# Kernel tuning notes

Hardware: AMD Instinct MI355X
Metric: run time of the kernel (lower is better)

## Reference

```python
import jax, jax.numpy as jnp
import numpy as np

N = 50000      # nodes
E = 800000     # directed edges (before self-loops)
FEAT = 120     # raw node feature dim
TOPO = 8       # topological feature dim
H1, D1 = 8, 8  # conv1: heads, per-head dim
C = 40         # out_channels (classes)
NEG_SLOPE = 0.2


def setup_inputs() -> dict:
    key = jax.random.key(0)
    ks = jax.random.split(key, 10)
    return {
        "x": jax.random.normal(ks[0], (N, FEAT), dtype=jnp.float32),
        "topo": jax.random.normal(ks[1], (N, TOPO), dtype=jnp.float32),
        "edge_index": jax.random.randint(ks[2], (2, E), 0, N, dtype=jnp.int32),
        "W1": jax.random.normal(ks[3], (FEAT + TOPO, H1 * D1), dtype=jnp.float32) * 0.1,
        "a_src1": jax.random.normal(ks[4], (H1, D1), dtype=jnp.float32) * 0.1,
        "a_dst1": jax.random.normal(ks[5], (H1, D1), dtype=jnp.float32) * 0.1,
        "b1": jnp.zeros((H1 * D1,), dtype=jnp.float32),
        "W2": jax.random.normal(ks[6], (H1 * D1, C), dtype=jnp.float32) * 0.1,
        "a_src2": jax.random.normal(ks[7], (1, C), dtype=jnp.float32) * 0.1,
        "a_dst2": jax.random.normal(ks[8], (1, C), dtype=jnp.float32) * 0.1,
        "b2": jnp.zeros((C,), dtype=jnp.float32),
    }


def gat_conv(x, src, dst, W, a_src, a_dst, b, heads, d, concat):
    """PyG-style GATConv (eval mode). src/dst already include self-loops."""
    n = x.shape[0]
    h = (x @ W).reshape(n, heads, d)                      # [N,H,D]
    al_src = jnp.sum(h * a_src[None], axis=-1)            # [N,H]
    al_dst = jnp.sum(h * a_dst[None], axis=-1)            # [N,H]
    e = jax.nn.leaky_relu(al_src[src] + al_dst[dst], NEG_SLOPE)  # [E',H]
    # segment softmax over incoming edges per destination node
    m = jax.ops.segment_max(e, dst, num_segments=n)       # [N,H]
    p = jnp.exp(e - m[dst])                               # [E',H]
    s = jax.ops.segment_sum(p, dst, num_segments=n)       # [N,H]
    alpha = p / s[dst]                                    # [E',H]
    out = jax.ops.segment_sum(alpha[:, :, None] * h[src], dst, num_segments=n)  # [N,H,D]
    if concat:
        return out.reshape(n, heads * d) + b
    return out.mean(axis=1) + b


def reference(x, topo, edge_index, W1, a_src1, a_dst1, b1, W2, a_src2, a_dst2, b2):
    n = x.shape[0]
    loops = jnp.arange(n, dtype=edge_index.dtype)
    src = jnp.concatenate([edge_index[0], loops])
    dst = jnp.concatenate([edge_index[1], loops])
    xin = jnp.concatenate([x, topo], axis=1)              # [N, FEAT+TOPO]
    h = jax.nn.elu(gat_conv(xin, src, dst, W1, a_src1, a_dst1, b1, H1, D1, True))
    out = gat_conv(h, src, dst, W2, a_src2, a_dst2, b2, 1, C, False)
    return jax.nn.log_softmax(out, axis=1)
```

## Files before the change

kernel.cpp:

```cpp
#include <hip/hip_runtime.h>
#include <hip/hip_fp16.h>

#define NN 50000
#define EE 800000
#define NBUCK 196
#define CAP 5120
#define TILEA 2048
#define NBA ((EE + TILEA - 1) / TILEA)
#define NGB 782
#define SRCS_MAX (EE + 8 * NN + 64)
#define LOG2E 1.4426950408889634f
#define PF 6

typedef _Float16 half8 __attribute__((ext_vector_type(8)));
typedef float floatx4 __attribute__((ext_vector_type(4)));
typedef float floatx2 __attribute__((ext_vector_type(2)));

__device__ __forceinline__ unsigned char f32_to_fp8(float a) {
    int r = __builtin_amdgcn_cvt_pk_fp8_f32(a, a, 0, false);
    return (unsigned char)(r & 0xff);
}
__device__ __forceinline__ float2 fp8pair_lo(unsigned v) {
    floatx2 r = __builtin_amdgcn_cvt_pk_f32_fp8(v, false);
    return make_float2(r[0], r[1]);
}
__device__ __forceinline__ float2 fp8pair_hi(unsigned v) {
    floatx2 r = __builtin_amdgcn_cvt_pk_f32_fp8(v, true);
    return make_float2(r[0], r[1]);
}
__device__ __forceinline__ float fexp2(float x) {
#if __has_builtin(__builtin_amdgcn_exp2f)
    return __builtin_amdgcn_exp2f(x);
#else
    return exp2f(x);
#endif
}
__device__ __forceinline__ float fexp(float x) {
    return fexp2(x * LOG2E);
}
__device__ __forceinline__ float flog(float x) {
#if __has_builtin(__builtin_amdgcn_logf)
    return 0.6931471805599453f * __builtin_amdgcn_logf(x);
#else
    return __logf(x);
#endif
}
__device__ __forceinline__ float frcp(float x) {
#if __has_builtin(__builtin_amdgcn_rcpf)
    return __builtin_amdgcn_rcpf(x);
#else
    return 1.f / x;
#endif
}

__global__ void k_prep(const float* __restrict__ W1, const float* __restrict__ W2,
                       _Float16* __restrict__ Bf1, _Float16* __restrict__ Bf2,
                       int* __restrict__ cursor, float* __restrict__ al2s,
                       unsigned char* __restrict__ pk1, __half* __restrict__ h2p) {
    int tid = blockIdx.x * 256 + threadIdx.x;
    if (tid < 1024) {
        int kk = tid >> 8, ct = (tid >> 6) & 3, L = tid & 63;
        int k0 = kk * 32 + (L >> 4) * 8, col = ct * 16 + (L & 15);
        half8 v;
        #pragma unroll
        for (int j = 0; j < 8; j++) v[j] = (_Float16)W1[(k0 + j) * 64 + col];
        *(half8*)(Bf1 + ((size_t)((kk * 4 + ct) * 64 + L)) * 8) = v;
    } else if (tid < 1024 + 384) {
        int u = tid - 1024;
        int kk = u / 192, rem = u % 192;
        int ct = rem >> 6, L = rem & 63;
        int k0 = kk * 32 + (L >> 4) * 8, col = ct * 16 + (L & 15);
        half8 v;
        #pragma unroll
        for (int j = 0; j < 8; j++)
            v[j] = (col < 40) ? (_Float16)W2[(k0 + j) * 40 + col] : (_Float16)0.f;
        *(half8*)(Bf2 + ((size_t)((kk * 3 + ct) * 64 + L)) * 8) = v;
    } else {
        int u = tid - 1408;
        if (u < NBUCK) cursor[u] = 0;
        if (u == 208) al2s[NN] = -1e30f;
        if (u >= 216 && u < 236) ((unsigned*)(h2p + (size_t)NN * 40))[u - 216] = 0u;
        if (u >= 240 && u < 272) {
            int dw = u - 240;
            ((float*)(pk1 + (size_t)NN * 128))[dw] = ((dw & 3) == 0) ? -1e30f : 0.f;
        }
    }
}

__global__ __launch_bounds__(256) void k_fusedAG(
    const int* __restrict__ ei, int* __restrict__ cursor,
    unsigned* __restrict__ bucketData,
    const float* __restrict__ x, const float* __restrict__ topo,
    const _Float16* __restrict__ Bf1,
    const float* __restrict__ a_src, const float* __restrict__ a_dst,
    unsigned char* __restrict__ pk1, float* __restrict__ aldst) {
    if (blockIdx.x < NBA) {
        __shared__ int cnt[NBUCK], base[NBUCK];
        int t = threadIdx.x;
        for (int i = t; i < NBUCK; i += 256) cnt[i] = 0;
        __syncthreads();
        int e0 = blockIdx.x * TILEA;
        int nE = min(TILEA, EE - e0);
        unsigned pk[8]; int bk[8], rk[8];
        int m = 0;
        for (int i = t; i < nE; i += 256) {
            int e = e0 + i;
            int s = ei[e], d = ei[EE + e];
            pk[m] = ((unsigned)d << 16) | (unsigned)s;
            bk[m] = d >> 8;
            rk[m] = atomicAdd(&cnt[bk[m]], 1);
            m++;
        }
        __syncthreads();
        for (int i = t; i < NBUCK; i += 256)
            base[i] = (cnt[i] > 0) ? atomicAdd(&cursor[i], cnt[i]) : 0;
        __syncthreads();
        for (int k = 0; k < m; k++) {
            int pos = base[bk[k]] + rk[k];
            if (pos < CAP) bucketData[(size_t)bk[k] * CAP + pos] = pk[k];
        }
        return;
    }
    int wave = threadIdx.x >> 6, lane = threadIdx.x & 63;
    int row0 = (blockIdx.x - NBA) * 64 + wave * 16;
    if (row0 >= NN) return;
    int g = lane >> 4, li = lane & 15;
    int myrow = row0 + li;
    half8 B[16];
    const half8* bp = (const half8*)Bf1;
    #pragma unroll
    for (int i = 0; i < 16; i++) B[i] = bp[i * 64 + lane];
    floatx4 acc[4] = {{0,0,0,0},{0,0,0,0},{0,0,0,0},{0,0,0,0}};
    #pragma unroll
    for (int kk = 0; kk < 4; kk++) {
        int k0 = kk * 32 + g * 8;
        const float* sp = (k0 == 120) ? (topo + (size_t)myrow * 8)
                                      : (x + (size_t)myrow * 120 + k0);
        float4 u0 = ((const float4*)sp)[0];
        float4 u1 = ((const float4*)sp)[1];
        half8 av;
        av[0] = (_Float16)u0.x; av[1] = (_Float16)u0.y;
        av[2] = (_Float16)u0.z; av[3] = (_Float16)u0.w;
        av[4] = (_Float16)u1.x; av[5] = (_Float16)u1.y;
        av[6] = (_Float16)u1.z; av[7] = (_Float16)u1.w;
        #pragma unroll
        for (int ct = 0; ct < 4; ct++)
            acc[ct] = __builtin_amdgcn_mfma_f32_16x16x32_f16(av, B[kk * 4 + ct], acc[ct], 0, 0, 0);
    }
    #pragma unroll
    for (int ct = 0; ct < 4; ct++)
        #pragma unroll
        for (int r = 0; r < 4; r++) {
            int col = ct * 16 + li;
            pk1[(size_t)(row0 + 4 * g + r) * 128 + (((col >> 3) << 4) + 4 + (col & 7))]
                = f32_to_fp8(acc[ct][r]);
        }
    float ps[4][4], pd[4][4];
    #pragma unroll
    for (int ct = 0; ct < 4; ct++) {
        int head = 2 * ct + (li >> 3), dix = li & 7;
        float asv = a_src[head * 8 + dix];
        float adv = a_dst[head * 8 + dix];
        #pragma unroll
        for (int r = 0; r < 4; r++) {
            ps[ct][r] = acc[ct][r] * asv;
            pd[ct][r] = acc[ct][r] * adv;
        }
    }
    #pragma unroll
    for (int off = 1; off <= 4; off <<= 1)
        #pragma unroll
        for (int ct = 0; ct < 4; ct++)
            #pragma unroll
            for (int r = 0; r < 4; r++) {
                ps[ct][r] += __shfl_xor(ps[ct][r], off, 64);
                pd[ct][r] += __shfl_xor(pd[ct][r], off, 64);
            }
    if ((li & 7) == 0) {
        #pragma unroll
        for (int ct = 0; ct < 4; ct++) {
            int head = 2 * ct + (li >> 3);
            #pragma unroll
            for (int r = 0; r < 4; r++) {
                int row = row0 + 4 * g + r;
                *(float*)(pk1 + (size_t)row * 128 + head * 16) = ps[ct][r] * LOG2E;
                aldst[row * 8 + head] = pd[ct][r] * LOG2E;
            }
        }
    }
}

__global__ __launch_bounds__(1024) void k_bucketB(const unsigned* __restrict__ bucketData,
        const int* __restrict__ cursor,
        int2* __restrict__ rowseg, int* __restrict__ srcs) {
    __shared__ int cnt[256], cur[256], sbuf[256], svals[256];
    __shared__ int sorted[CAP + 2048];
    int b = blockIdx.x, t = threadIdx.x;
    int nloc = min(256, NN - b * 256);
    int ecnt = min(cursor[b], CAP);
    size_t inBase = (size_t)b * CAP;
    if (t < 256) {
        int vv = 0;
        if (t < NBUCK) {
            int nl = min(256, NN - t * 256);
            vv = min(cursor[t], CAP) + 8 * nl;
        }
        svals[t] = vv;
    }
    __syncthreads();
    int* a = svals; int* bb = sbuf;
    for (int off = 1; off < 256; off <<= 1) {
        if (t < 256) bb[t] = a[t] + ((t >= off) ? a[t - off] : 0);
        __syncthreads();
        int* tmp = a; a = bb; bb = tmp;
    }
    int outBase = (b == 0) ? 0 : a[b - 1];
    __syncthreads();
    if (t < 256) cnt[t] = (t < nloc) ? 1 : 0;
    __syncthreads();
    for (int i = t; i < ecnt; i += 1024) {
        unsigned u = bucketData[inBase + i];
        atomicAdd(&cnt[(u >> 16) & 255], 1);
    }
    __syncthreads();
    int cv = 0, pcv = 0;
    if (t < 256) {
        cv = cnt[t];
        pcv = (t < nloc) ? ((cv + 7) & ~7) : 0;
        sbuf[t] = pcv;
    }
    __syncthreads();
    a = sbuf; bb = cnt;
    for (int off = 1; off < 256; off <<= 1) {
        if (t < 256) bb[t] = a[t] + ((t >= off) ? a[t - off] : 0);
        __syncthreads();
        int* tmp = a; a = bb; bb = tmp;
    }
    int total = a[255];
    int excl = (t < 256) ? (a[t] - pcv) : 0;
    __syncthreads();
    if (t < nloc) {
        rowseg[b * 256 + t] = make_int2(outBase + excl, outBase + excl + pcv);
        sorted[excl] = b * 256 + t;
        for (int k = cv; k < pcv; k++) sorted[excl + k] = NN;
        cur[t] = excl + 1;
    }
    __syncthreads();
    for (int i = t; i < ecnt; i += 1024) {
        unsigned u = bucketData[inBase + i];
        int ld = (u >> 16) & 255;
        int p = atomicAdd(&cur[ld], 1);
        sorted[p] = (int)(u & 0xffffu);
    }
    __syncthreads();
    for (int i = t; i < total; i += 1024) srcs[outBase + i] = sorted[i];
}

__global__ __launch_bounds__(256) void k_agg1(
    const int2* __restrict__ rowseg, const int* __restrict__ srcs,
    const unsigned char* __restrict__ pk1, const float* __restrict__ aldst,
    const float* __restrict__ b1, __half* __restrict__ hout) {
    int wave = threadIdx.x >> 6;
    int lane = threadIdx.x & 63;
    int d = blockIdx.x * 4 + wave;
    if (d >= NN) return;
    int eh = lane >> 3;
    int cq = lane & 7;
    unsigned cq16 = (unsigned)cq << 4;
    float adst = aldst[d * 8 + cq];
    int2 seg = rowseg[d];
    int jb = seg.x, je = seg.y;
    int niter = (je - jb) >> 3;
    int idx[PF];
    #pragma unroll
    for (int k = 0; k < PF; k++) {
        int jj = min(jb + 8 * k, je - 8);
        idx[k] = srcs[jj + eh];
    }
    uint4 qv[PF];
    #pragma unroll
    for (int k = 0; k < PF; k++)
        qv[k] = *(const uint4*)(pk1 + (((unsigned)idx[k] << 7) | cq16));
    float c0 = 0.f, c1 = 0.f, c2 = 0.f, c3 = 0.f;
    float c4 = 0.f, c5 = 0.f, c6 = 0.f, c7 = 0.f, ssum = 0.f;
    #pragma unroll
    for (int k = 0; k < PF; k++) {
        if (k >= niter) break;
        float e = __uint_as_float(qv[k].x) + adst;
        float p = fexp2(fmaxf(e, 0.2f * e));
        float2 f0 = fp8pair_lo(qv[k].y), f1 = fp8pair_hi(qv[k].y);
        float2 f2 = fp8pair_lo(qv[k].z), f3 = fp8pair_hi(qv[k].z);
        ssum += p;
        c0 += p * f0.x; c1 += p * f0.y;
        c2 += p * f1.x; c3 += p * f1.y;
        c4 += p * f2.x; c5 += p * f2.y;
        c6 += p * f3.x; c7 += p * f3.y;
    }
    for (int j = jb + 8 * PF; j < je; j += 8) {
        int sn = srcs[j + eh];
        uint4 q = *(const uint4*)(pk1 + (((unsigned)sn << 7) | cq16));
        float e = __uint_as_float(q.x) + adst;
        float p = fexp2(fmaxf(e, 0.2f * e));
        float2 f0 = fp8pair_lo(q.y), f1 = fp8pair_hi(q.y);
        float2 f2 = fp8pair_lo(q.z), f3 = fp8pair_hi(q.z);
        ssum += p;
        c0 += p * f0.x; c1 += p * f0.y;
        c2 += p * f1.x; c3 += p * f1.y;
        c4 += p * f2.x; c5 += p * f2.y;
        c6 += p * f3.x; c7 += p * f3.y;
    }
    #pragma unroll
    for (int off = 8; off <= 32; off <<= 1) {
        ssum += __shfl_xor(ssum, off, 64);
        c0 += __shfl_xor(c0, off, 64); c1 += __shfl_xor(c1, off, 64);
        c2 += __shfl_xor(c2, off, 64); c3 += __shfl_xor(c3, off, 64);
        c4 += __shfl_xor(c4, off, 64); c5 += __shfl_xor(c5, off, 64);
        c6 += __shfl_xor(c6, off, 64); c7 += __shfl_xor(c7, off, 64);
    }
    if (eh == 0) {
        float4 bl = ((const float4*)b1)[2 * cq];
        float4 bh = ((const float4*)b1)[2 * cq + 1];
        float inv = frcp(ssum);
        float v0 = c0 * inv + bl.x, v1 = c1 * inv + bl.y;
        float v2 = c2 * inv + bl.z, v3 = c3 * inv + bl.w;
        float v4 = c4 * inv + bh.x, v5 = c5 * inv + bh.y;
        float v6 = c6 * inv + bh.z, v7 = c7 * inv + bh.w;
        v0 = (v0 > 0.f) ? v0 : (fexp(v0) - 1.f);
        v1 = (v1 > 0.f) ? v1 : (fexp(v1) - 1.f);
        v2 = (v2 > 0.f) ? v2 : (fexp(v2) - 1.f);
        v3 = (v3 > 0.f) ? v3 : (fexp(v3) - 1.f);
        v4 = (v4 > 0.f) ? v4 : (fexp(v4) - 1.f);
        v5 = (v5 > 0.f) ? v5 : (fexp(v5) - 1.f);
        v6 = (v6 > 0.f) ? v6 : (fexp(v6) - 1.f);
        v7 = (v7 > 0.f) ? v7 : (fexp(v7) - 1.f);
        __half2 p0 = __floats2half2_rn(v0, v1);
        __half2 p1 = __floats2half2_rn(v2, v3);
        __half2 p2 = __floats2half2_rn(v4, v5);
        __half2 p3 = __floats2half2_rn(v6, v7);
        uint4 pk;
        pk.x = *(unsigned*)&p0; pk.y = *(unsigned*)&p1;
        pk.z = *(unsigned*)&p2; pk.w = *(unsigned*)&p3;
        *(uint4*)(hout + (size_t)d * 64 + 8 * cq) = pk;
    }
}

__global__ __launch_bounds__(256) void k_gemm2(
    const __half* __restrict__ hout, const _Float16* __restrict__ Bf2,
    const float* __restrict__ a_src2, const float* __restrict__ a_dst2,
    __half* __restrict__ h2p, float* __restrict__ al2s, float* __restrict__ al2d) {
    int wave = threadIdx.x >> 6, lane = threadIdx.x & 63;
    int row0 = blockIdx.x * 64 + wave * 16;
    if (row0 >= NN) return;
    int g = lane >> 4, li = lane & 15;
    int myrow = row0 + li;
    half8 B[6];
    const half8* bp = (const half8*)Bf2;
    #pragma unroll
    for (int i = 0; i < 6; i++) B[i] = bp[i * 64 + lane];
    floatx4 acc[3] = {{0,0,0,0},{0,0,0,0},{0,0,0,0}};
    #pragma unroll
    for (int kk = 0; kk < 2; kk++) {
        int k0 = kk * 32 + g * 8;
        half8 av = *(const half8*)(hout + (size_t)myrow * 64 + k0);
        #pragma unroll
        for (int ct = 0; ct < 3; ct++)
            acc[ct] = __builtin_amdgcn_mfma_f32_16x16x32_f16(av, B[kk * 3 + ct], acc[ct], 0, 0, 0);
    }
    float ts[4] = {0.f, 0.f, 0.f, 0.f}, td[4] = {0.f, 0.f, 0.f, 0.f};
    #pragma unroll
    for (int ct = 0; ct < 3; ct++) {
        int col = ct * 16 + li;
        bool ok = (col < 40);
        float asv = ok ? a_src2[col] : 0.f;
        float adv = ok ? a_dst2[col] : 0.f;
        #pragma unroll
        for (int r = 0; r < 4; r++) {
            ts[r] += acc[ct][r] * asv;
            td[r] += acc[ct][r] * adv;
            if (ok) h2p[(size_t)(row0 + 4 * g + r) * 40 + col] = __float2half(acc[ct][r]);
        }
    }
    #pragma unroll
    for (int off = 1; off <= 8; off <<= 1)
        #pragma unroll
        for (int r = 0; r < 4; r++) {
            ts[r] += __shfl_xor(ts[r], off, 64);
            td[r] += __shfl_xor(td[r], off, 64);
        }
    if (li == 0) {
        #pragma unroll
        for (int r = 0; r < 4; r++) {
            int row = row0 + 4 * g + r;
            al2s[row] = ts[r] * LOG2E;
            al2d[row] = td[r] * LOG2E;
        }
    }
}

__global__ __launch_bounds__(256) void k_agg2(
    const int2* __restrict__ rowseg, const int* __restrict__ srcs,
    const float* __restrict__ al2s, const float* __restrict__ al2d,
    const __half* __restrict__ h2p, const float* __restrict__ b2,
    float* __restrict__ out) {
    int wave = threadIdx.x >> 6;
    int lane = threadIdx.x & 63;
    int d = blockIdx.x * 4 + wave;
    if (d >= NN) return;
    int eh = lane >> 3;
    int cq = lane & 7;
    bool act = (cq < 5);
    int cqc = act ? cq : 4;
    unsigned cq16 = (unsigned)cqc << 4;
    const char* H = (const char*)h2p;
    float adst = al2d[d];
    int2 seg = rowseg[d];
    int jb = seg.x, je = seg.y;
    int niter = (je - jb) >> 3;
    int idx[PF];
    #pragma unroll
    for (int k = 0; k < PF; k++) {
        int jj = min(jb + 8 * k, je - 8);
        idx[k] = srcs[jj + eh];
    }
    float alv[PF]; uint4 qv[PF];
    #pragma unroll
    for (int k = 0; k < PF; k++) {
        alv[k] = al2s[idx[k]];
        qv[k]  = *(const uint4*)(H + ((unsigned)idx[k] * 80u + cq16));
    }
    float c0 = 0.f, c1 = 0.f, c2 = 0.f, c3 = 0.f;
    float c4 = 0.f, c5 = 0.f, c6 = 0.f, c7 = 0.f, ssum = 0.f;
    #pragma unroll
    for (int k = 0; k < PF; k++) {
        if (k >= niter) break;
        float e = alv[k] + adst;
        float p = fexp2(fmaxf(e, 0.2f * e));
        float2 f0 = __half22float2(*(__half2*)&qv[k].x);
        float2 f1 = __half22float2(*(__half2*)&qv[k].y);
        float2 f2 = __half22float2(*(__half2*)&qv[k].z);
        float2 f3 = __half22float2(*(__half2*)&qv[k].w);
        ssum += p;
        c0 += p * f0.x; c1 += p * f0.y;
        c2 += p * f1.x; c3 += p * f1.y;
        c4 += p * f2.x; c5 += p * f2.y;
        c6 += p * f3.x; c7 += p * f3.y;
    }
    for (int j = jb + 8 * PF; j < je; j += 8) {
        int sn = srcs[j + eh];
        float al = al2s[sn];
        uint4 q = *(const uint4*)(H + ((unsigned)sn * 80u + cq16));
        float e = al + adst;
        float p = fexp2(fmaxf(e, 0.2f * e));
        float2 f0 = __half22float2(*(__half2*)&q.x);
        float2 f1 = __half22float2(*(__half2*)&q.y);
        float2 f2 = __half22float2(*(__half2*)&q.z);
        float2 f3 = __half22float2(*(__half2*)&q.w);
        ssum += p;
        c0 += p * f0.x; c1 += p * f0.y;
        c2 += p * f1.x; c3 += p * f1.y;
        c4 += p * f2.x; c5 += p * f2.y;
        c6 += p * f3.x; c7 += p * f3.y;
    }
    #pragma unroll
    for (int off = 8; off <= 32; off <<= 1) {
        ssum += __shfl_xor(ssum, off, 64);
        c0 += __shfl_xor(c0, off, 64); c1 += __shfl_xor(c1, off, 64);
        c2 += __shfl_xor(c2, off, 64); c3 += __shfl_xor(c3, off, 64);
        c4 += __shfl_xor(c4, off, 64); c5 += __shfl_xor(c5, off, 64);
        c6 += __shfl_xor(c6, off, 64); c7 += __shfl_xor(c7, off, 64);
    }
    float inv = frcp(ssum);
    float4 bl = ((const float4*)b2)[2 * cqc];
    float4 bh = ((const float4*)b2)[2 * cqc + 1];
    float o0 = c0 * inv + bl.x, o1 = c1 * inv + bl.y;
    float o2 = c2 * inv + bl.z, o3 = c3 * inv + bl.w;
    float o4 = c4 * inv + bh.x, o5 = c5 * inv + bh.y;
    float o6 = c6 * inv + bh.z, o7 = c7 * inv + bh.w;
    float mo = act ? fmaxf(fmaxf(fmaxf(o0, o1), fmaxf(o2, o3)),
                           fmaxf(fmaxf(o4, o5), fmaxf(o6, o7))) : -3.0e38f;
    #pragma unroll
    for (int off = 1; off <= 4; off <<= 1) mo = fmaxf(mo, __shfl_xor(mo, off, 64));
    float te = act ? (fexp(o0 - mo) + fexp(o1 - mo) + fexp(o2 - mo) + fexp(o3 - mo) +
                      fexp(o4 - mo) + fexp(o5 - mo) + fexp(o6 - mo) + fexp(o7 - mo)) : 0.f;
    #pragma unroll
    for (int off = 1; off <= 4; off <<= 1) te += __shfl_xor(te, off, 64);
    float ls = mo + flog(te);
    if (act && eh == 0) {
        float4 lo = make_float4(o0 - ls, o1 - ls, o2 - ls, o3 - ls);
        float4 hi = make_float4(o4 - ls, o5 - ls, o6 - ls, o7 - ls);
        *(float4*)(out + (size_t)d * 40 + 8 * cq) = lo;
        *(float4*)(out + (size_t)d * 40 + 8 * cq + 4) = hi;
    }
}

extern "C" void kernel_launch(void* const* d_in, const int* in_sizes, int n_in,
                              void* d_out, int out_size, void* d_ws, size_t ws_size,
                              hipStream_t stream) {
    (void)in_sizes; (void)n_in; (void)out_size; (void)ws_size;
    const float* x    = (const float*)d_in[0];
    const float* topo = (const float*)d_in[1];
    const int*   ei   = (const int*)d_in[2];
    const float* W1   = (const float*)d_in[3];
    const float* as1  = (const float*)d_in[4];
    const float* ad1  = (const float*)d_in[5];
    const float* b1   = (const float*)d_in[6];
    const float* W2   = (const float*)d_in[7];
    const float* as2  = (const float*)d_in[8];
    const float* ad2  = (const float*)d_in[9];
    const float* b2   = (const float*)d_in[10];
    float* out = (float*)d_out;

    char* ws = (char*)d_ws;
    size_t off = 0;
    auto alloc = [&](size_t bytes) {
        void* p = ws + off;
        off += (bytes + 255) / 256 * 256;
        return p;
    };
    int2*          rowseg     = (int2*)alloc((size_t)NN * 8);
    int*           cursor     = (int*)alloc(NBUCK * 4);
    unsigned*      bucketData = (unsigned*)alloc((size_t)NBUCK * CAP * 4);
    int*           srcs       = (int*)alloc((size_t)SRCS_MAX * 4);
    float*         aldst1     = (float*)alloc((size_t)NN * 8 * 4);
    float*         al2s       = (float*)alloc((NN + 1) * 4);
    float*         al2d       = (float*)alloc(NN * 4);
    _Float16*      Bf1        = (_Float16*)alloc(4 * 4 * 64 * 8 * 2);
    _Float16*      Bf2        = (_Float16*)alloc(2 * 3 * 64 * 8 * 2);
    unsigned char* pk1        = (unsigned char*)alloc((size_t)(NN + 1) * 128);
    __half*        hout       = (__half*)alloc((size_t)NN * 64 * 2);
    __half*        h2p        = (__half*)alloc((size_t)(NN + 1) * 40 * 2);

    k_prep    <<<7,         256,  0, stream>>>(W1, W2, Bf1, Bf2, cursor, al2s, pk1, h2p);
    k_fusedAG <<<NBA + NGB, 256,  0, stream>>>(ei, cursor, bucketData,
                                               x, topo, Bf1, as1, ad1, pk1, aldst1);
    k_bucketB <<<NBUCK,     1024, 0, stream>>>(bucketData, cursor, rowseg, srcs);
    k_agg1    <<<(NN + 3) / 4, 256, 0, stream>>>(rowseg, srcs, pk1, aldst1, b1, hout);
    k_gemm2   <<<782,       256,  0, stream>>>(hout, Bf2, as2, ad2, h2p, al2s, al2d);
    k_agg2    <<<(NN + 3) / 4, 256, 0, stream>>>(rowseg, srcs, al2s, al2d, h2p, b2, out);
}
```

Measured before the change: 176.3 us.

## Map one lane per feature channel in aggregation kernels, reorganize packed row layout

Both aggregation kernels switch from 8 edges × 8 channels per wave with cross-lane reductions to each lane owning one output channel and walking all edges four at a time with software prefetch. The packed layer-1 row layout is reorganized so the 8 per-head attention logits come first, followed by 64 contiguous fp8 values. This removes the shuffle reductions and per-lane vector unpacking, at the cost of many narrow per-lane byte/short gathers and redundant exp computation per lane. Segments are assumed padded to multiples of 4.

```diff
diff --git a/kernel.cpp b/kernel.cpp
--- a/kernel.cpp
+++ b/kernel.cpp
@@ -10,7 +10,6 @@
 #define NGB 782
 #define SRCS_MAX (EE + 8 * NN + 64)
 #define LOG2E 1.4426950408889634f
-#define PF 6
 
 typedef _Float16 half8 __attribute__((ext_vector_type(8)));
 typedef float floatx4 __attribute__((ext_vector_type(4)));
@@ -20,13 +19,9 @@
     int r = __builtin_amdgcn_cvt_pk_fp8_f32(a, a, 0, false);
     return (unsigned char)(r & 0xff);
 }
-__device__ __forceinline__ float2 fp8pair_lo(unsigned v) {
+__device__ __forceinline__ float fp8_byte0_to_f32(unsigned v) {
     floatx2 r = __builtin_amdgcn_cvt_pk_f32_fp8(v, false);
-    return make_float2(r[0], r[1]);
-}
-__device__ __forceinline__ float2 fp8pair_hi(unsigned v) {
-    floatx2 r = __builtin_amdgcn_cvt_pk_f32_fp8(v, true);
-    return make_float2(r[0], r[1]);
+    return r[0];
 }
 __device__ __forceinline__ float fexp2(float x) {
 #if __has_builtin(__builtin_amdgcn_exp2f)
@@ -80,9 +75,9 @@
         if (u < NBUCK) cursor[u] = 0;
         if (u == 208) al2s[NN] = -1e30f;
         if (u >= 216 && u < 236) ((unsigned*)(h2p + (size_t)NN * 40))[u - 216] = 0u;
-        if (u >= 240 && u < 272) {
+        if (u >= 240 && u < 264) {
             int dw = u - 240;
-            ((float*)(pk1 + (size_t)NN * 128))[dw] = ((dw & 3) == 0) ? -1e30f : 0.f;
+            ((float*)(pk1 + (size_t)NN * 128))[dw] = (dw < 8) ? -1e30f : 0.f;
         }
     }
 }
@@ -152,8 +147,7 @@
         #pragma unroll
         for (int r = 0; r < 4; r++) {
             int col = ct * 16 + li;
-            pk1[(size_t)(row0 + 4 * g + r) * 128 + (((col >> 3) << 4) + 4 + (col & 7))]
-                = f32_to_fp8(acc[ct][r]);
+            pk1[(size_t)(row0 + 4 * g + r) * 128 + 32 + col] = f32_to_fp8(acc[ct][r]);
         }
     float ps[4][4], pd[4][4];
     #pragma unroll
@@ -183,7 +177,7 @@
             #pragma unroll
             for (int r = 0; r < 4; r++) {
                 int row = row0 + 4 * g + r;
-                *(float*)(pk1 + (size_t)row * 128 + head * 16) = ps[ct][r] * LOG2E;
+                *(float*)(pk1 + (size_t)row * 128 + head * 4) = ps[ct][r] * LOG2E;
                 aldst[row * 8 + head] = pd[ct][r] * LOG2E;
             }
         }
@@ -264,84 +258,51 @@
     int lane = threadIdx.x & 63;
     int d = blockIdx.x * 4 + wave;
     if (d >= NN) return;
-    int eh = lane >> 3;
-    int cq = lane & 7;
-    unsigned cq16 = (unsigned)cq << 4;
-    float adst = aldst[d * 8 + cq];
+    int head = lane >> 3;
+    unsigned alOff = (unsigned)head << 2;
+    unsigned vOff = 32u + (unsigned)lane;
+    float adst = aldst[d * 8 + head];
     int2 seg = rowseg[d];
-    int jb = seg.x, je = seg.y;
-    int niter = (je - jb) >> 3;
-    int idx[PF];
-    #pragma unroll
-    for (int k = 0; k < PF; k++) {
-        int jj = min(jb + 8 * k, je - 8);
-        idx[k] = srcs[jj + eh];
-    }
-    uint4 qv[PF];
-    #pragma unroll
-    for (int k = 0; k < PF; k++)
-        qv[k] = *(const uint4*)(pk1 + (((unsigned)idx[k] << 7) | cq16));
-    float c0 = 0.f, c1 = 0.f, c2 = 0.f, c3 = 0.f;
-    float c4 = 0.f, c5 = 0.f, c6 = 0.f, c7 = 0.f, ssum = 0.f;
-    #pragma unroll
-    for (int k = 0; k < PF; k++) {
-        if (k >= niter) break;
-        float e = __uint_as_float(qv[k].x) + adst;
-        float p = fexp2(fmaxf(e, 0.2f * e));
-        float2 f0 = fp8pair_lo(qv[k].y), f1 = fp8pair_hi(qv[k].y);
-        float2 f2 = fp8pair_lo(qv[k].z), f3 = fp8pair_hi(qv[k].z);
-        ssum += p;
-        c0 += p * f0.x; c1 += p * f0.y;
-        c2 += p * f1.x; c3 += p * f1.y;
-        c4 += p * f2.x; c5 += p * f2.y;
-        c6 += p * f3.x; c7 += p * f3.y;
-    }
-    for (int j = jb + 8 * PF; j < je; j += 8) {
-        int sn = srcs[j + eh];
-        uint4 q = *(const uint4*)(pk1 + (((unsigned)sn << 7) | cq16));
-        float e = __uint_as_float(q.x) + adst;
-        float p = fexp2(fmaxf(e, 0.2f * e));
-        float2 f0 = fp8pair_lo(q.y), f1 = fp8pair_hi(q.y);
-        float2 f2 = fp8pair_lo(q.z), f3 = fp8pair_hi(q.z);
-        ssum += p;
-        c0 += p * f0.x; c1 += p * f0.y;
-        c2 += p * f1.x; c3 += p * f1.y;
-        c4 += p * f2.x; c5 += p * f2.y;
-        c6 += p * f3.x; c7 += p * f3.y;
-    }
-    #pragma unroll
-    for (int off = 8; off <= 32; off <<= 1) {
-        ssum += __shfl_xor(ssum, off, 64);
-        c0 += __shfl_xor(c0, off, 64); c1 += __shfl_xor(c1, off, 64);
-        c2 += __shfl_xor(c2, off, 64); c3 += __shfl_xor(c3, off, 64);
-        c4 += __shfl_xor(c4, off, 64); c5 += __shfl_xor(c5, off, 64);
-        c6 += __shfl_xor(c6, off, 64); c7 += __shfl_xor(c7, off, 64);
-    }
-    if (eh == 0) {
-        float4 bl = ((const float4*)b1)[2 * cq];
-        float4 bh = ((const float4*)b1)[2 * cq + 1];
-        float inv = frcp(ssum);
-        float v0 = c0 * inv + bl.x, v1 = c1 * inv + bl.y;
-        float v2 = c2 * inv + bl.z, v3 = c3 * inv + bl.w;
-        float v4 = c4 * inv + bh.x, v5 = c5 * inv + bh.y;
-        float v6 = c6 * inv + bh.z, v7 = c7 * inv + bh.w;
-        v0 = (v0 > 0.f) ? v0 : (fexp(v0) - 1.f);
-        v1 = (v1 > 0.f) ? v1 : (fexp(v1) - 1.f);
-        v2 = (v2 > 0.f) ? v2 : (fexp(v2) - 1.f);
-        v3 = (v3 > 0.f) ? v3 : (fexp(v3) - 1.f);
-        v4 = (v4 > 0.f) ? v4 : (fexp(v4) - 1.f);
-        v5 = (v5 > 0.f) ? v5 : (fexp(v5) - 1.f);
-        v6 = (v6 > 0.f) ? v6 : (fexp(v6) - 1.f);
-        v7 = (v7 > 0.f) ? v7 : (fexp(v7) - 1.f);
-        __half2 p0 = __floats2half2_rn(v0, v1);
-        __half2 p1 = __floats2half2_rn(v2, v3);
-        __half2 p2 = __floats2half2_rn(v4, v5);
-        __half2 p3 = __floats2half2_rn(v6, v7);
-        uint4 pk;
-        pk.x = *(unsigned*)&p0; pk.y = *(unsigned*)&p1;
-        pk.z = *(unsigned*)&p2; pk.w = *(unsigned*)&p3;
-        *(uint4*)(hout + (size_t)d * 64 + 8 * cq) = pk;
-    }
+    int jb = __builtin_amdgcn_readfirstlane(seg.x);
+    int je = __builtin_amdgcn_readfirstlane(seg.y);
+    const int* sp = srcs + jb;
+    int ng = (je - jb) >> 2;
+    float c = 0.f, ssum = 0.f;
+    int4 iA = *(const int4*)sp;
+    float a0, a1, a2, a3; unsigned v0, v1, v2, v3;
+    {
+        const unsigned char* r0 = pk1 + ((size_t)(unsigned)iA.x << 7);
+        const unsigned char* r1 = pk1 + ((size_t)(unsigned)iA.y << 7);
+        const unsigned char* r2 = pk1 + ((size_t)(unsigned)iA.z << 7);
+        const unsigned char* r3 = pk1 + ((size_t)(unsigned)iA.w << 7);
+        a0 = *(const float*)(r0 + alOff); v0 = r0[vOff];
+        a1 = *(const float*)(r1 + alOff); v1 = r1[vOff];
+        a2 = *(const float*)(r2 + alOff); v2 = r2[vOff];
+        a3 = *(const float*)(r3 + alOff); v3 = r3[vOff];
+    }
+    for (int g = 0; g < ng; g++) {
+        int gn = (g + 1 < ng) ? g + 1 : g;
+        int4 iB = *(const int4*)(sp + 4 * gn);
+        const unsigned char* r0 = pk1 + ((size_t)(unsigned)iB.x << 7);
+        const unsigned char* r1 = pk1 + ((size_t)(unsigned)iB.y << 7);
+        const unsigned char* r2 = pk1 + ((size_t)(unsigned)iB.z << 7);
+        const unsigned char* r3 = pk1 + ((size_t)(unsigned)iB.w << 7);
+        float n0 = *(const float*)(r0 + alOff); unsigned w0 = r0[vOff];
+        float n1 = *(const float*)(r1 + alOff); unsigned w1 = r1[vOff];
+        float n2 = *(const float*)(r2 + alOff); unsigned w2 = r2[vOff];
+        float n3 = *(const float*)(r3 + alOff); unsigned w3 = r3[vOff];
+        float e, p;
+        e = a0 + adst; p = fexp2(fmaxf(e, 0.2f * e)); ssum += p; c += p * fp8_byte0_to_f32(v0);
+        e = a1 + adst; p = fexp2(fmaxf(e, 0.2f * e)); ssum += p; c += p * fp8_byte0_to_f32(v1);
+        e = a2 + adst; p = fexp2(fmaxf(e, 0.2f * e)); ssum += p; c += p * fp8_byte0_to_f32(v2);
+        e = a3 + adst; p = fexp2(fmaxf(e, 0.2f * e)); ssum += p; c += p * fp8_byte0_to_f32(v3);
+        a0 = n0; a1 = n1; a2 = n2; a3 = n3;
+        v0 = w0; v1 = w1; v2 = w2; v3 = w3;
+    }
+    float inv = frcp(ssum);
+    float vo = c * inv + b1[lane];
+    vo = (vo > 0.f) ? vo : (fexp(vo) - 1.f);
+    hout[(size_t)d * 64 + lane] = __float2half(vo);
 }
 
 __global__ __launch_bounds__(256) void k_gemm2(
@@ -406,91 +367,49 @@
     int lane = threadIdx.x & 63;
     int d = blockIdx.x * 4 + wave;
     if (d >= NN) return;
-    int eh = lane >> 3;
-    int cq = lane & 7;
-    bool act = (cq < 5);
-    int cqc = act ? cq : 4;
-    unsigned cq16 = (unsigned)cqc << 4;
+    bool act = (lane < 40);
+    unsigned vOff = 2u * (unsigned)(act ? lane : 39);
     const char* H = (const char*)h2p;
     float adst = al2d[d];
     int2 seg = rowseg[d];
-    int jb = seg.x, je = seg.y;
-    int niter = (je - jb) >> 3;
-    int idx[PF];
-    #pragma unroll
-    for (int k = 0; k < PF; k++) {
-        int jj = min(jb + 8 * k, je - 8);
-        idx[k] = srcs[jj + eh];
-    }
-    float alv[PF]; uint4 qv[PF];
-    #pragma unroll
-    for (int k = 0; k < PF; k++) {
-        alv[k] = al2s[idx[k]];
-        qv[k]  = *(const uint4*)(H + ((unsigned)idx[k] * 80u + cq16));
-    }
-    float c0 = 0.f, c1 = 0.f, c2 = 0.f, c3 = 0.f;
-    float c4 = 0.f, c5 = 0.f, c6 = 0.f, c7 = 0.f, ssum = 0.f;
-    #pragma unroll
-    for (int k = 0; k < PF; k++) {
-        if (k >= niter) break;
-        float e = alv[k] + adst;
-        float p = fexp2(fmaxf(e, 0.2f * e));
-        float2 f0 = __half22float2(*(__half2*)&qv[k].x);
-        float2 f1 = __half22float2(*(__half2*)&qv[k].y);
-        float2 f2 = __half22float2(*(__half2*)&qv[k].z);
-        float2 f3 = __half22float2(*(__half2*)&qv[k].w);
-        ssum += p;
-        c0 += p * f0.x; c1 += p * f0.y;
-        c2 += p * f1.x; c3 += p * f1.y;
-        c4 += p * f2.x; c5 += p * f2.y;
-        c6 += p * f3.x; c7 += p * f3.y;
-    }
-    for (int j = jb + 8 * PF; j < je; j += 8) {
-        int sn = srcs[j + eh];
-        float al = al2s[sn];
-        uint4 q = *(const uint4*)(H + ((unsigned)sn * 80u + cq16));
-        float e = al + adst;
-        float p = fexp2(fmaxf(e, 0.2f * e));
-        float2 f0 = __half22float2(*(__half2*)&q.x);
-        float2 f1 = __half22float2(*(__half2*)&q.y);
-        float2 f2 = __half22float2(*(__half2*)&q.z);
-        float2 f3 = __half22float2(*(__half2*)&q.w);
-        ssum += p;
-        c0 += p * f0.x; c1 += p * f0.y;
-        c2 += p * f1.x; c3 += p * f1.y;
-        c4 += p * f2.x; c5 += p * f2.y;
-        c6 += p * f3.x; c7 += p * f3.y;
-    }
-    #pragma unroll
-    for (int off = 8; off <= 32; off <<= 1) {
-        ssum += __shfl_xor(ssum, off, 64);
-        c0 += __shfl_xor(c0, off, 64); c1 += __shfl_xor(c1, off, 64);
-        c2 += __shfl_xor(c2, off, 64); c3 += __shfl_xor(c3, off, 64);
-        c4 += __shfl_xor(c4, off, 64); c5 += __shfl_xor(c5, off, 64);
-        c6 += __shfl_xor(c6, off, 64); c7 += __shfl_xor(c7, off, 64);
+    int jb = __builtin_amdgcn_readfirstlane(seg.x);
+    int je = __builtin_amdgcn_readfirstlane(seg.y);
+    const int* sp = srcs + jb;
+    int ng = (je - jb) >> 2;
+    float c = 0.f, ssum = 0.f;
+    int4 iA = *(const int4*)sp;
+    float a0, a1, a2, a3; unsigned short v0, v1, v2, v3;
+    {
+        a0 = al2s[iA.x]; v0 = *(const unsigned short*)(H + (unsigned)iA.x * 80u + vOff);
+        a1 = al2s[iA.y]; v1 = *(const unsigned short*)(H + (unsigned)iA.y * 80u + vOff);
+        a2 = al2s[iA.z]; v2 = *(const unsigned short*)(H + (unsigned)iA.z * 80u + vOff);
+        a3 = al2s[iA.w]; v3 = *(const unsigned short*)(H + (unsigned)iA.w * 80u + vOff);
+    }
+    for (int g = 0; g < ng; g++) {
+        int gn = (g + 1 < ng) ? g + 1 : g;
+        int4 iB = *(const int4*)(sp + 4 * gn);
+        float n0 = al2s[iB.x]; unsigned short w0 = *(const unsigned short*)(H + (unsigned)iB.x * 80u + vOff);
+        float n1 = al2s[iB.y]; unsigned short w1 = *(const unsigned short*)(H + (unsigned)iB.y * 80u + vOff);
+        float n2 = al2s[iB.z]; unsigned short w2 = *(const unsigned short*)(H + (unsigned)iB.z * 80u + vOff);
+        float n3 = al2s[iB.w]; unsigned short w3 = *(const unsigned short*)(H + (unsigned)iB.w * 80u + vOff);
+        float e, p;
+        e = a0 + adst; p = fexp2(fmaxf(e, 0.2f * e)); ssum += p; c += p * __half2float(*(__half*)&v0);
+        e = a1 + adst; p = fexp2(fmaxf(e, 0.2f * e)); ssum += p; c += p * __half2float(*(__half*)&v1);
+        e = a2 + adst; p = fexp2(fmaxf(e, 0.2f * e)); ssum += p; c += p * __half2float(*(__half*)&v2);
+        e = a3 + adst; p = fexp2(fmaxf(e, 0.2f * e)); ssum += p; c += p * __half2float(*(__half*)&v3);
+        a0 = n0; a1 = n1; a2 = n2; a3 = n3;
+        v0 = w0; v1 = w1; v2 = w2; v3 = w3;
     }
     float inv = frcp(ssum);
-    float4 bl = ((const float4*)b2)[2 * cqc];
-    float4 bh = ((const float4*)b2)[2 * cqc + 1];
-    float o0 = c0 * inv + bl.x, o1 = c1 * inv + bl.y;
-    float o2 = c2 * inv + bl.z, o3 = c3 * inv + bl.w;
-    float o4 = c4 * inv + bh.x, o5 = c5 * inv + bh.y;
-    float o6 = c6 * inv + bh.z, o7 = c7 * inv + bh.w;
-    float mo = act ? fmaxf(fmaxf(fmaxf(o0, o1), fmaxf(o2, o3)),
-                           fmaxf(fmaxf(o4, o5), fmaxf(o6, o7))) : -3.0e38f;
-    #pragma unroll
-    for (int off = 1; off <= 4; off <<= 1) mo = fmaxf(mo, __shfl_xor(mo, off, 64));
-    float te = act ? (fexp(o0 - mo) + fexp(o1 - mo) + fexp(o2 - mo) + fexp(o3 - mo) +
-                      fexp(o4 - mo) + fexp(o5 - mo) + fexp(o6 - mo) + fexp(o7 - mo)) : 0.f;
-    #pragma unroll
-    for (int off = 1; off <= 4; off <<= 1) te += __shfl_xor(te, off, 64);
+    float o = act ? (c * inv + b2[act ? lane : 0]) : -3.0e38f;
+    float mo = o;
+    #pragma unroll
+    for (int off = 1; off <= 32; off <<= 1) mo = fmaxf(mo, __shfl_xor(mo, off, 64));
+    float te = act ? fexp(o - mo) : 0.f;
+    #pragma unroll
+    for (int off = 1; off <= 32; off <<= 1) te += __shfl_xor(te, off, 64);
     float ls = mo + flog(te);
-    if (act && eh == 0) {
-        float4 lo = make_float4(o0 - ls, o1 - ls, o2 - ls, o3 - ls);
-        float4 hi = make_float4(o4 - ls, o5 - ls, o6 - ls, o7 - ls);
-        *(float4*)(out + (size_t)d * 40 + 8 * cq) = lo;
-        *(float4*)(out + (size_t)d * 40 + 8 * cq + 4) = hi;
-    }
+    if (act) out[(size_t)d * 40 + lane] = o - ls;
 }
 
 extern "C" void kernel_launch(void* const* d_in, const int* in_sizes, int n_in,
```

Result: slower. 187.9 us (+6.6%).
